# Kernel tuning notes

Hardware: AMD Instinct MI355X
Metric: run time of the kernel (lower is better)

The kernel has to match this reference:

```python
import jax, jax.numpy as jnp
import numpy as np

B, TAPE, N, F = 128, 100000, 50000, 32

def setup_inputs() -> dict:
    key = jax.random.key(0)
    k1, k2, k3, k4 = jax.random.split(key, 4)
    tape = jax.random.normal(k1, (B, TAPE), dtype=jnp.float32)
    input_indices = jax.random.randint(k2, (N, F), 0, TAPE)
    # He init scaled by fan-in, padding slots (index==0) zeroed as in __init__
    weights = jax.random.normal(k3, (N, F), dtype=jnp.float32) * jnp.sqrt(2.0 / F)
    weights = jnp.where(input_indices == 0, 0.0, weights)
    bias = jnp.zeros((N,), dtype=jnp.float32)
    output_indices = jnp.arange(N)
    act_type = jax.random.randint(k4, (N,), 0, 2)
    return {"tape": tape, "weights": weights, "bias": bias,
            "input_indices": input_indices, "output_indices": output_indices,
            "act_type": act_type}

def reference(tape, weights, bias, input_indices, output_indices, act_type):
    # gather padded fan-in inputs: [B, N, F]
    gathered = tape[:, input_indices]
    # weighted sum over fan-in + bias: [B, N]
    x = jnp.einsum('bnf,nf->bn', gathered, weights) + bias
    # per-activation-type apply (two activation groups: relu / tanh)
    x = jnp.where(act_type == 0, jax.nn.relu(x), jnp.tanh(x))
    # scatter results back into tape
    return tape.at[:, output_indices].set(x)
```

## Files before the change

kernel.cpp:

```cpp
#include <hip/hip_runtime.h>
#include <cmath>

#define TAPE_SZ 100000
#define N_SZ    50000
#define F_SZ    32
#define B_SZ    128
#define NGRP    8
#define GSUB    16
#define NBV     128
#define NCHUNK  ((N_SZ + NBV - 1) / NBV)
#define NGATHER (NCHUNK * NGRP)
#define NTAIL   512
#define TAIL_F4 1600000

static __device__ __forceinline__ unsigned short f32_to_bf16(float f) {
    unsigned int u = __float_as_uint(f);
    u = (u + 0x7fffu + ((u >> 16) & 1u)) >> 16;
    return (unsigned short)u;
}

__global__ __launch_bounds__(256) void transpose_tape(const float* __restrict__ in,
                                                      unsigned short* __restrict__ outT) {
    __shared__ float tile[32][129];
    const int x0 = blockIdx.x * 32;
    const int tx = threadIdx.x;
    const int ty = threadIdx.y;

    #pragma unroll
    for (int yy = ty; yy < B_SZ; yy += 8)
        tile[tx][yy] = in[(size_t)yy * TAPE_SZ + x0 + tx];
    __syncthreads();

    const int tid = ty * 32 + tx;
    const int g = tid >> 5;
    const int l = tid & 31;
    unsigned short* dst = outT + ((size_t)g * TAPE_SZ + x0 + l) * GSUB;
    union { unsigned short u[8]; uint4 q; } p0, p1;
    #pragma unroll
    for (int k = 0; k < 8; ++k) {
        p0.u[k] = f32_to_bf16(tile[l][g * GSUB + k]);
        p1.u[k] = f32_to_bf16(tile[l][g * GSUB + 8 + k]);
    }
    *(uint4*)dst       = p0.q;
    *(uint4*)(dst + 8) = p1.q;
}

__global__ __launch_bounds__(256) void gather_mm(const unsigned short* __restrict__ tapeT,
                                                 const float* __restrict__ weights,
                                                 const float* __restrict__ bias,
                                                 const int*   __restrict__ in_idx,
                                                 const int*   __restrict__ out_idx,
                                                 const int*   __restrict__ act_type,
                                                 const float* __restrict__ tape,
                                                 float* __restrict__ out) {
    __shared__ int   s_idx[NBV][33];
    __shared__ float s_w[NBV][33];
    __shared__ float s_bias[NBV];
    __shared__ int   s_act[NBV];
    __shared__ int   s_oidx[NBV];
    __shared__ float s_x[GSUB][132];

    const int tid = threadIdx.x;

    if (blockIdx.x >= NGATHER) {
        const float4* src = (const float4*)tape;
        float4*       dst = (float4*)out;
        const int stride = NTAIL * 256;
        for (int i = (blockIdx.x - NGATHER) * 256 + tid; i < TAIL_F4; i += stride) {
            const int b = i / 12500;
            const int j = i - b * 12500;
            const int off = b * (TAPE_SZ / 4) + (N_SZ / 4) + j;
            dst[off] = src[off];
        }
        return;
    }

    const int g     = blockIdx.x & (NGRP - 1);
    const int chunk = blockIdx.x >> 3;
    const int n0    = chunk * NBV;
    const int nend  = min(NBV, N_SZ - n0);

    for (int t = tid; t < nend * 32; t += 256) {
        const int n = t >> 5, f = t & 31;
        s_idx[n][f] = in_idx[(size_t)n0 * 32 + t];
        s_w[n][f]   = weights[(size_t)n0 * 32 + t];
    }
    if (tid < nend) {
        s_bias[tid] = bias[n0 + tid];
        s_act[tid]  = act_type[n0 + tid];
        s_oidx[tid] = out_idx[n0 + tid];
    }
    __syncthreads();

    const int nl   = tid >> 1;
    const int half = tid & 1;
    const unsigned short* tg = tapeT + (size_t)g * TAPE_SZ * GSUB + half * 8;

    if (nl < nend) {
        float a0 = 0.f, a1 = 0.f, a2 = 0.f, a3 = 0.f, a4 = 0.f, a5 = 0.f, a6 = 0.f, a7 = 0.f;

        #pragma unroll
        for (int fo = 0; fo < 32; fo += 8) {
            int   i8[8]; float w8[8];
            #pragma unroll
            for (int j = 0; j < 8; ++j) { i8[j] = s_idx[nl][fo + j]; w8[j] = s_w[nl][fo + j]; }
            uint4 q8[8];
            #pragma unroll
            for (int j = 0; j < 8; ++j)
                q8[j] = *(const uint4*)(tg + (size_t)i8[j] * GSUB);
            #pragma unroll
            for (int j = 0; j < 8; ++j) {
                const float w = w8[j];
                a0 = fmaf(__uint_as_float(q8[j].x << 16),         w, a0);
                a1 = fmaf(__uint_as_float(q8[j].x & 0xffff0000u), w, a1);
                a2 = fmaf(__uint_as_float(q8[j].y << 16),         w, a2);
                a3 = fmaf(__uint_as_float(q8[j].y & 0xffff0000u), w, a3);
                a4 = fmaf(__uint_as_float(q8[j].z << 16),         w, a4);
                a5 = fmaf(__uint_as_float(q8[j].z & 0xffff0000u), w, a5);
                a6 = fmaf(__uint_as_float(q8[j].w << 16),         w, a6);
                a7 = fmaf(__uint_as_float(q8[j].w & 0xffff0000u), w, a7);
            }
        }

        const float bz = s_bias[nl];
        a0 += bz; a1 += bz; a2 += bz; a3 += bz; a4 += bz; a5 += bz; a6 += bz; a7 += bz;
        if (s_act[nl] == 0) {
            a0 = fmaxf(a0, 0.f); a1 = fmaxf(a1, 0.f); a2 = fmaxf(a2, 0.f); a3 = fmaxf(a3, 0.f);
            a4 = fmaxf(a4, 0.f); a5 = fmaxf(a5, 0.f); a6 = fmaxf(a6, 0.f); a7 = fmaxf(a7, 0.f);
        } else {
            a0 = tanhf(a0); a1 = tanhf(a1); a2 = tanhf(a2); a3 = tanhf(a3);
            a4 = tanhf(a4); a5 = tanhf(a5); a6 = tanhf(a6); a7 = tanhf(a7);
        }
        const int bs = half * 8;
        s_x[bs + 0][nl] = a0; s_x[bs + 1][nl] = a1; s_x[bs + 2][nl] = a2; s_x[bs + 3][nl] = a3;
        s_x[bs + 4][nl] = a4; s_x[bs + 5][nl] = a5; s_x[bs + 6][nl] = a6; s_x[bs + 7][nl] = a7;
    }
    __syncthreads();

    const int quads = (nend + 3) >> 2;
    for (int idx = tid; idx < GSUB * quads; idx += 256) {
        int bsub, j4;
        if (nend == NBV) { bsub = idx >> 5; j4 = idx & 31; }
        else             { bsub = idx / quads; j4 = idx - bsub * quads; }
        const int nq  = j4 * 4;
        const int oc0 = s_oidx[nq];
        float* orow = out + (size_t)(g * GSUB + bsub) * TAPE_SZ;
        const bool consec = (nq + 3 < nend) &&
                            (s_oidx[nq + 1] == oc0 + 1) &&
                            (s_oidx[nq + 2] == oc0 + 2) &&
                            (s_oidx[nq + 3] == oc0 + 3) && ((oc0 & 3) == 0);
        if (consec) {
            *(float4*)(orow + oc0) = make_float4(s_x[bsub][nq + 0], s_x[bsub][nq + 1],
                                                 s_x[bsub][nq + 2], s_x[bsub][nq + 3]);
        } else {
            #pragma unroll
            for (int c = 0; c < 4; ++c)
                if (nq + c < nend) orow[s_oidx[nq + c]] = s_x[bsub][nq + c];
        }
    }
}

__global__ __launch_bounds__(128) void gather_fallback(const float* __restrict__ tape,
                                                       const float* __restrict__ weights,
                                                       const float* __restrict__ bias,
                                                       const int*   __restrict__ in_idx,
                                                       const int*   __restrict__ out_idx,
                                                       const int*   __restrict__ act_type,
                                                       float* __restrict__ out) {
    const int n = blockIdx.x;
    const int b = threadIdx.x;
    float acc = 0.f;
    for (int f = 0; f < F_SZ; ++f) {
        acc += tape[(size_t)b * TAPE_SZ + in_idx[(size_t)n * F_SZ + f]] *
               weights[(size_t)n * F_SZ + f];
    }
    acc += bias[n];
    acc = (act_type[n] == 0) ? fmaxf(acc, 0.f) : tanhf(acc);
    out[(size_t)b * TAPE_SZ + out_idx[n]] = acc;
}

__global__ __launch_bounds__(256) void copy_tail_fb(const float* __restrict__ tape,
                                                    float* __restrict__ out) {
    const int n4 = (TAPE_SZ - N_SZ) / 4;
    int i = blockIdx.x * blockDim.x + threadIdx.x;
    int b = blockIdx.y;
    if (i < n4) {
        const float4* src = (const float4*)(tape + (size_t)b * TAPE_SZ + N_SZ);
        float4*       dst = (float4*)(out  + (size_t)b * TAPE_SZ + N_SZ);
        dst[i] = src[i];
    }
}

extern "C" void kernel_launch(void* const* d_in, const int* in_sizes, int n_in,
                              void* d_out, int out_size, void* d_ws, size_t ws_size,
                              hipStream_t stream) {
    const float* tape    = (const float*)d_in[0];
    const float* weights = (const float*)d_in[1];
    const float* bias    = (const float*)d_in[2];
    const int*   in_idx  = (const int*)d_in[3];
    const int*   out_idx = (const int*)d_in[4];
    const int*   act     = (const int*)d_in[5];
    float*       out     = (float*)d_out;

    const size_t need = (size_t)TAPE_SZ * B_SZ * sizeof(unsigned short);
    if (ws_size >= need) {
        unsigned short* tapeT = (unsigned short*)d_ws;
        transpose_tape<<<dim3(TAPE_SZ / 32), dim3(32, 8), 0, stream>>>(tape, tapeT);
        gather_mm<<<dim3(NGATHER + NTAIL), dim3(256), 0, stream>>>(
            tapeT, weights, bias, in_idx, out_idx, act, tape, out);
    } else {
        copy_tail_fb<<<dim3(((TAPE_SZ - N_SZ) / 4 + 255) / 256, B_SZ), 256, 0, stream>>>(tape, out);
        gather_fallback<<<dim3(N_SZ), 128, 0, stream>>>(
            tape, weights, bias, in_idx, out_idx, act, out);
    }
}
```

Measured before the change: 188.5 us.

## Halve neurons per block, split batch across four threads, pack index/weight in LDS

Each block now handles 64 neurons instead of 128, and each neuron's 16-batch group is split across four threads. Each thread does 8-byte gathers and keeps four accumulators instead of eight. Indices and weights are interleaved as int2 in shared memory, and the output staging buffer aliases that array behind an extra barrier. Launch bounds request 8 blocks per CU. Together these cut registers and LDS per block to raise occupancy and memory-level parallelism for the random gathers, at the cost of smaller per-thread loads and twice as many blocks.

```diff
diff --git a/kernel.cpp b/kernel.cpp
--- a/kernel.cpp
+++ b/kernel.cpp
@@ -7,7 +7,7 @@
 #define B_SZ    128
 #define NGRP    8
 #define GSUB    16
-#define NBV     128
+#define NBV     64
 #define NCHUNK  ((N_SZ + NBV - 1) / NBV)
 #define NGATHER (NCHUNK * NGRP)
 #define NTAIL   512
@@ -45,20 +45,19 @@
     *(uint4*)(dst + 8) = p1.q;
 }
 
-__global__ __launch_bounds__(256) void gather_mm(const unsigned short* __restrict__ tapeT,
-                                                 const float* __restrict__ weights,
-                                                 const float* __restrict__ bias,
-                                                 const int*   __restrict__ in_idx,
-                                                 const int*   __restrict__ out_idx,
-                                                 const int*   __restrict__ act_type,
-                                                 const float* __restrict__ tape,
-                                                 float* __restrict__ out) {
-    __shared__ int   s_idx[NBV][33];
-    __shared__ float s_w[NBV][33];
+__global__ __launch_bounds__(256, 8) void gather_mm(const unsigned short* __restrict__ tapeT,
+                                                    const float* __restrict__ weights,
+                                                    const float* __restrict__ bias,
+                                                    const int*   __restrict__ in_idx,
+                                                    const int*   __restrict__ out_idx,
+                                                    const int*   __restrict__ act_type,
+                                                    const float* __restrict__ tape,
+                                                    float* __restrict__ out) {
+    __shared__ int2  s_iw[NBV][33];
     __shared__ float s_bias[NBV];
     __shared__ int   s_act[NBV];
     __shared__ int   s_oidx[NBV];
-    __shared__ float s_x[GSUB][132];
+    float (*s_x)[68] = (float (*)[68])&s_iw[0][0];
 
     const int tid = threadIdx.x;
 
@@ -82,8 +81,8 @@
 
     for (int t = tid; t < nend * 32; t += 256) {
         const int n = t >> 5, f = t & 31;
-        s_idx[n][f] = in_idx[(size_t)n0 * 32 + t];
-        s_w[n][f]   = weights[(size_t)n0 * 32 + t];
+        s_iw[n][f] = make_int2(in_idx[(size_t)n0 * 32 + t],
+                               __float_as_int(weights[(size_t)n0 * 32 + t]));
     }
     if (tid < nend) {
         s_bias[tid] = bias[n0 + tid];
@@ -92,55 +91,52 @@
     }
     __syncthreads();
 
-    const int nl   = tid >> 1;
-    const int half = tid & 1;
-    const unsigned short* tg = tapeT + (size_t)g * TAPE_SZ * GSUB + half * 8;
-
+    const int nl = tid >> 2;
+    const int q  = tid & 3;
+    const unsigned short* tg = tapeT + (size_t)g * TAPE_SZ * GSUB + q * 4;
+
+    float a0 = 0.f, a1 = 0.f, a2 = 0.f, a3 = 0.f;
     if (nl < nend) {
-        float a0 = 0.f, a1 = 0.f, a2 = 0.f, a3 = 0.f, a4 = 0.f, a5 = 0.f, a6 = 0.f, a7 = 0.f;
-
         #pragma unroll
         for (int fo = 0; fo < 32; fo += 8) {
-            int   i8[8]; float w8[8];
-            #pragma unroll
-            for (int j = 0; j < 8; ++j) { i8[j] = s_idx[nl][fo + j]; w8[j] = s_w[nl][fo + j]; }
-            uint4 q8[8];
+            int2 iw8[8];
+            #pragma unroll
+            for (int j = 0; j < 8; ++j) iw8[j] = s_iw[nl][fo + j];
+            uint2 q8[8];
             #pragma unroll
             for (int j = 0; j < 8; ++j)
-                q8[j] = *(const uint4*)(tg + (size_t)i8[j] * GSUB);
+                q8[j] = *(const uint2*)(tg + (size_t)iw8[j].x * GSUB);
             #pragma unroll
             for (int j = 0; j < 8; ++j) {
-                const float w = w8[j];
+                const float w = __int_as_float(iw8[j].y);
                 a0 = fmaf(__uint_as_float(q8[j].x << 16),         w, a0);
                 a1 = fmaf(__uint_as_float(q8[j].x & 0xffff0000u), w, a1);
                 a2 = fmaf(__uint_as_float(q8[j].y << 16),         w, a2);
                 a3 = fmaf(__uint_as_float(q8[j].y & 0xffff0000u), w, a3);
-                a4 = fmaf(__uint_as_float(q8[j].z << 16),         w, a4);
-                a5 = fmaf(__uint_as_float(q8[j].z & 0xffff0000u), w, a5);
-                a6 = fmaf(__uint_as_float(q8[j].w << 16),         w, a6);
-                a7 = fmaf(__uint_as_float(q8[j].w & 0xffff0000u), w, a7);
             }
         }
-
         const float bz = s_bias[nl];
-        a0 += bz; a1 += bz; a2 += bz; a3 += bz; a4 += bz; a5 += bz; a6 += bz; a7 += bz;
+        a0 += bz; a1 += bz; a2 += bz; a3 += bz;
         if (s_act[nl] == 0) {
-            a0 = fmaxf(a0, 0.f); a1 = fmaxf(a1, 0.f); a2 = fmaxf(a2, 0.f); a3 = fmaxf(a3, 0.f);
-            a4 = fmaxf(a4, 0.f); a5 = fmaxf(a5, 0.f); a6 = fmaxf(a6, 0.f); a7 = fmaxf(a7, 0.f);
+            a0 = fmaxf(a0, 0.f); a1 = fmaxf(a1, 0.f);
+            a2 = fmaxf(a2, 0.f); a3 = fmaxf(a3, 0.f);
         } else {
             a0 = tanhf(a0); a1 = tanhf(a1); a2 = tanhf(a2); a3 = tanhf(a3);
-            a4 = tanhf(a4); a5 = tanhf(a5); a6 = tanhf(a6); a7 = tanhf(a7);
-        }
-        const int bs = half * 8;
-        s_x[bs + 0][nl] = a0; s_x[bs + 1][nl] = a1; s_x[bs + 2][nl] = a2; s_x[bs + 3][nl] = a3;
-        s_x[bs + 4][nl] = a4; s_x[bs + 5][nl] = a5; s_x[bs + 6][nl] = a6; s_x[bs + 7][nl] = a7;
+        }
+    }
+    __syncthreads();
+
+    if (nl < nend) {
+        const int bs = q * 4;
+        s_x[bs + 0][nl] = a0; s_x[bs + 1][nl] = a1;
+        s_x[bs + 2][nl] = a2; s_x[bs + 3][nl] = a3;
     }
     __syncthreads();
 
     const int quads = (nend + 3) >> 2;
     for (int idx = tid; idx < GSUB * quads; idx += 256) {
         int bsub, j4;
-        if (nend == NBV) { bsub = idx >> 5; j4 = idx & 31; }
+        if (nend == NBV) { bsub = idx >> 4; j4 = idx & 15; }
         else             { bsub = idx / quads; j4 = idx - bsub * quads; }
         const int nq  = j4 * 4;
         const int oc0 = s_oidx[nq];
```

After: 187.8 us. About the same (-0.4%).

## Use full-row bf16 tape layout, fuse tail copy into transpose, shrink gather blocks

Applied to the files above, without the earlier changes.

The transposed bf16 tape changes from 8 batch groups of 16 to one contiguous 128-wide row per tape column. Each gathered index then reads a contiguous 256-byte row shared by 16 threads, replacing eight separate 32-byte reads spread across groups. The tail copy of untouched tape columns moves into the transpose kernel, which already holds that data in shared memory, so the extra copy blocks in the gather kernel go away. Gather blocks now handle 16 neurons across all 128 batches, and output writes are float4 across neurons for each batch row, which gives narrower store segments per row.

```diff
diff --git a/kernel.cpp b/kernel.cpp
--- a/kernel.cpp
+++ b/kernel.cpp
@@ -5,13 +5,8 @@
 #define N_SZ    50000
 #define F_SZ    32
 #define B_SZ    128
-#define NGRP    8
-#define GSUB    16
-#define NBV     128
-#define NCHUNK  ((N_SZ + NBV - 1) / NBV)
-#define NGATHER (NCHUNK * NGRP)
-#define NTAIL   512
-#define TAIL_F4 1600000
+#define NB      16
+#define NGATHER 3125
 
 static __device__ __forceinline__ unsigned short f32_to_bf16(float f) {
     unsigned int u = __float_as_uint(f);
@@ -20,7 +15,8 @@
 }
 
 __global__ __launch_bounds__(256) void transpose_tape(const float* __restrict__ in,
-                                                      unsigned short* __restrict__ outT) {
+                                                      unsigned short* __restrict__ outT,
+                                                      float* __restrict__ out) {
     __shared__ float tile[32][129];
     const int x0 = blockIdx.x * 32;
     const int tx = threadIdx.x;
@@ -32,17 +28,23 @@
     __syncthreads();
 
     const int tid = ty * 32 + tx;
-    const int g = tid >> 5;
-    const int l = tid & 31;
-    unsigned short* dst = outT + ((size_t)g * TAPE_SZ + x0 + l) * GSUB;
-    union { unsigned short u[8]; uint4 q; } p0, p1;
+    const int oct = tid & 15;
+    const int xl0 = tid >> 4;
     #pragma unroll
-    for (int k = 0; k < 8; ++k) {
-        p0.u[k] = f32_to_bf16(tile[l][g * GSUB + k]);
-        p1.u[k] = f32_to_bf16(tile[l][g * GSUB + 8 + k]);
+    for (int xx = xl0; xx < 32; xx += 16) {
+        const float* src = &tile[xx][oct * 8];
+        union { unsigned short u[8]; uint4 q; } pk;
+        #pragma unroll
+        for (int k = 0; k < 8; ++k)
+            pk.u[k] = f32_to_bf16(src[k]);
+        *(uint4*)(outT + (size_t)(x0 + xx) * B_SZ + oct * 8) = pk.q;
     }
-    *(uint4*)dst       = p0.q;
-    *(uint4*)(dst + 8) = p1.q;
+
+    if (x0 + tx >= N_SZ) {
+        #pragma unroll
+        for (int yy = ty; yy < B_SZ; yy += 8)
+            out[(size_t)yy * TAPE_SZ + x0 + tx] = tile[tx][yy];
+    }
 }
 
 __global__ __launch_bounds__(256) void gather_mm(const unsigned short* __restrict__ tapeT,
@@ -51,111 +53,91 @@
                                                  const int*   __restrict__ in_idx,
                                                  const int*   __restrict__ out_idx,
                                                  const int*   __restrict__ act_type,
-                                                 const float* __restrict__ tape,
                                                  float* __restrict__ out) {
-    __shared__ int   s_idx[NBV][33];
-    __shared__ float s_w[NBV][33];
-    __shared__ float s_bias[NBV];
-    __shared__ int   s_act[NBV];
-    __shared__ int   s_oidx[NBV];
-    __shared__ float s_x[GSUB][132];
+    __shared__ int   s_idx[NB][33];
+    __shared__ float s_w[NB][33];
+    __shared__ float s_bias[NB];
+    __shared__ int   s_act[NB];
+    __shared__ int   s_oidx[NB];
+    __shared__ float s_x[NB][132];
 
     const int tid = threadIdx.x;
+    const int n0 = blockIdx.x * NB;
 
-    if (blockIdx.x >= NGATHER) {
-        const float4* src = (const float4*)tape;
-        float4*       dst = (float4*)out;
-        const int stride = NTAIL * 256;
-        for (int i = (blockIdx.x - NGATHER) * 256 + tid; i < TAIL_F4; i += stride) {
-            const int b = i / 12500;
-            const int j = i - b * 12500;
-            const int off = b * (TAPE_SZ / 4) + (N_SZ / 4) + j;
-            dst[off] = src[off];
-        }
-        return;
-    }
-
-    const int g     = blockIdx.x & (NGRP - 1);
-    const int chunk = blockIdx.x >> 3;
-    const int n0    = chunk * NBV;
-    const int nend  = min(NBV, N_SZ - n0);
-
-    for (int t = tid; t < nend * 32; t += 256) {
+    #pragma unroll
+    for (int t = tid; t < NB * 32; t += 256) {
         const int n = t >> 5, f = t & 31;
         s_idx[n][f] = in_idx[(size_t)n0 * 32 + t];
         s_w[n][f]   = weights[(size_t)n0 * 32 + t];
     }
-    if (tid < nend) {
+    if (tid < NB) {
         s_bias[tid] = bias[n0 + tid];
         s_act[tid]  = act_type[n0 + tid];
         s_oidx[tid] = out_idx[n0 + tid];
     }
     __syncthreads();
 
-    const int nl   = tid >> 1;
-    const int half = tid & 1;
-    const unsigned short* tg = tapeT + (size_t)g * TAPE_SZ * GSUB + half * 8;
+    const int nl = tid >> 4;
+    const int bx = tid & 15;
+    float a0 = 0.f, a1 = 0.f, a2 = 0.f, a3 = 0.f, a4 = 0.f, a5 = 0.f, a6 = 0.f, a7 = 0.f;
 
-    if (nl < nend) {
-        float a0 = 0.f, a1 = 0.f, a2 = 0.f, a3 = 0.f, a4 = 0.f, a5 = 0.f, a6 = 0.f, a7 = 0.f;
+    #pragma unroll
+    for (int fo = 0; fo < 32; fo += 8) {
+        int   i8[8]; float w8[8];
+        #pragma unroll
+        for (int j = 0; j < 8; ++j) { i8[j] = s_idx[nl][fo + j]; w8[j] = s_w[nl][fo + j]; }
+        uint4 q8[8];
+        #pragma unroll
+        for (int j = 0; j < 8; ++j)
+            q8[j] = *(const uint4*)(tapeT + (size_t)i8[j] * B_SZ + bx * 8);
+        #pragma unroll
+        for (int j = 0; j < 8; ++j) {
+            const float w = w8[j];
+            a0 = fmaf(__uint_as_float(q8[j].x << 16),         w, a0);
+            a1 = fmaf(__uint_as_float(q8[j].x & 0xffff0000u), w, a1);
+            a2 = fmaf(__uint_as_float(q8[j].y << 16),         w, a2);
+            a3 = fmaf(__uint_as_float(q8[j].y & 0xffff0000u), w, a3);
+            a4 = fmaf(__uint_as_float(q8[j].z << 16),         w, a4);
+            a5 = fmaf(__uint_as_float(q8[j].z & 0xffff0000u), w, a5);
+            a6 = fmaf(__uint_as_float(q8[j].w << 16),         w, a6);
+            a7 = fmaf(__uint_as_float(q8[j].w & 0xffff0000u), w, a7);
+        }
+    }
 
-        #pragma unroll
-        for (int fo = 0; fo < 32; fo += 8) {
-            int   i8[8]; float w8[8];
-            #pragma unroll
-            for (int j = 0; j < 8; ++j) { i8[j] = s_idx[nl][fo + j]; w8[j] = s_w[nl][fo + j]; }
-            uint4 q8[8];
-            #pragma unroll
-            for (int j = 0; j < 8; ++j)
-                q8[j] = *(const uint4*)(tg + (size_t)i8[j] * GSUB);
-            #pragma unroll
-            for (int j = 0; j < 8; ++j) {
-                const float w = w8[j];
-                a0 = fmaf(__uint_as_float(q8[j].x << 16),         w, a0);
-                a1 = fmaf(__uint_as_float(q8[j].x & 0xffff0000u), w, a1);
-                a2 = fmaf(__uint_as_float(q8[j].y << 16),         w, a2);
-                a3 = fmaf(__uint_as_float(q8[j].y & 0xffff0000u), w, a3);
-                a4 = fmaf(__uint_as_float(q8[j].z << 16),         w, a4);
-                a5 = fmaf(__uint_as_float(q8[j].z & 0xffff0000u), w, a5);
-                a6 = fmaf(__uint_as_float(q8[j].w << 16),         w, a6);
-                a7 = fmaf(__uint_as_float(q8[j].w & 0xffff0000u), w, a7);
-            }
-        }
-
-        const float bz = s_bias[nl];
-        a0 += bz; a1 += bz; a2 += bz; a3 += bz; a4 += bz; a5 += bz; a6 += bz; a7 += bz;
-        if (s_act[nl] == 0) {
-            a0 = fmaxf(a0, 0.f); a1 = fmaxf(a1, 0.f); a2 = fmaxf(a2, 0.f); a3 = fmaxf(a3, 0.f);
-            a4 = fmaxf(a4, 0.f); a5 = fmaxf(a5, 0.f); a6 = fmaxf(a6, 0.f); a7 = fmaxf(a7, 0.f);
-        } else {
-            a0 = tanhf(a0); a1 = tanhf(a1); a2 = tanhf(a2); a3 = tanhf(a3);
-            a4 = tanhf(a4); a5 = tanhf(a5); a6 = tanhf(a6); a7 = tanhf(a7);
-        }
-        const int bs = half * 8;
-        s_x[bs + 0][nl] = a0; s_x[bs + 1][nl] = a1; s_x[bs + 2][nl] = a2; s_x[bs + 3][nl] = a3;
-        s_x[bs + 4][nl] = a4; s_x[bs + 5][nl] = a5; s_x[bs + 6][nl] = a6; s_x[bs + 7][nl] = a7;
+    const float bz = s_bias[nl];
+    a0 += bz; a1 += bz; a2 += bz; a3 += bz; a4 += bz; a5 += bz; a6 += bz; a7 += bz;
+    if (s_act[nl] == 0) {
+        a0 = fmaxf(a0, 0.f); a1 = fmaxf(a1, 0.f); a2 = fmaxf(a2, 0.f); a3 = fmaxf(a3, 0.f);
+        a4 = fmaxf(a4, 0.f); a5 = fmaxf(a5, 0.f); a6 = fmaxf(a6, 0.f); a7 = fmaxf(a7, 0.f);
+    } else {
+        a0 = tanhf(a0); a1 = tanhf(a1); a2 = tanhf(a2); a3 = tanhf(a3);
+        a4 = tanhf(a4); a5 = tanhf(a5); a6 = tanhf(a6); a7 = tanhf(a7);
+    }
+    {
+        const int b8 = bx * 8;
+        s_x[nl][b8 + 0] = a0; s_x[nl][b8 + 1] = a1; s_x[nl][b8 + 2] = a2; s_x[nl][b8 + 3] = a3;
+        s_x[nl][b8 + 4] = a4; s_x[nl][b8 + 5] = a5; s_x[nl][b8 + 6] = a6; s_x[nl][b8 + 7] = a7;
     }
     __syncthreads();
 
-    const int quads = (nend + 3) >> 2;
-    for (int idx = tid; idx < GSUB * quads; idx += 256) {
-        int bsub, j4;
-        if (nend == NBV) { bsub = idx >> 5; j4 = idx & 31; }
-        else             { bsub = idx / quads; j4 = idx - bsub * quads; }
-        const int nq  = j4 * 4;
-        const int oc0 = s_oidx[nq];
-        float* orow = out + (size_t)(g * GSUB + bsub) * TAPE_SZ;
-        const bool consec = (nq + 3 < nend) &&
-                            (s_oidx[nq + 1] == oc0 + 1) &&
-                            (s_oidx[nq + 2] == oc0 + 2) &&
-                            (s_oidx[nq + 3] == oc0 + 3) && ((oc0 & 3) == 0);
+    const int g  = tid >> 6;
+    const int b0 = tid & 63;
+    const int oc0 = s_oidx[g * 4];
+    const bool consec = (s_oidx[g * 4 + 1] == oc0 + 1) &&
+                        (s_oidx[g * 4 + 2] == oc0 + 2) &&
+                        (s_oidx[g * 4 + 3] == oc0 + 3) && ((oc0 & 3) == 0);
+    #pragma unroll
+    for (int rep = 0; rep < 2; ++rep) {
+        const int b = b0 + rep * 64;
+        const float4 v = make_float4(s_x[g * 4 + 0][b], s_x[g * 4 + 1][b],
+                                     s_x[g * 4 + 2][b], s_x[g * 4 + 3][b]);
         if (consec) {
-            *(float4*)(orow + oc0) = make_float4(s_x[bsub][nq + 0], s_x[bsub][nq + 1],
-                                                 s_x[bsub][nq + 2], s_x[bsub][nq + 3]);
+            *(float4*)(out + (size_t)b * TAPE_SZ + oc0) = v;
         } else {
-            #pragma unroll
-            for (int c = 0; c < 4; ++c)
-                if (nq + c < nend) orow[s_oidx[nq + c]] = s_x[bsub][nq + c];
+            out[(size_t)b * TAPE_SZ + s_oidx[g * 4 + 0]] = v.x;
+            out[(size_t)b * TAPE_SZ + s_oidx[g * 4 + 1]] = v.y;
+            out[(size_t)b * TAPE_SZ + s_oidx[g * 4 + 2]] = v.z;
+            out[(size_t)b * TAPE_SZ + s_oidx[g * 4 + 3]] = v.w;
         }
     }
 }
@@ -205,9 +187,9 @@
     const size_t need = (size_t)TAPE_SZ * B_SZ * sizeof(unsigned short);
     if (ws_size >= need) {
         unsigned short* tapeT = (unsigned short*)d_ws;
-        transpose_tape<<<dim3(TAPE_SZ / 32), dim3(32, 8), 0, stream>>>(tape, tapeT);
-        gather_mm<<<dim3(NGATHER + NTAIL), dim3(256), 0, stream>>>(
-            tapeT, weights, bias, in_idx, out_idx, act, tape, out);
+        transpose_tape<<<dim3(TAPE_SZ / 32), dim3(32, 8), 0, stream>>>(tape, tapeT, out);
+        gather_mm<<<dim3(NGATHER), dim3(256), 0, stream>>>(
+            tapeT, weights, bias, in_idx, out_idx, act, out);
     } else {
         copy_tail_fb<<<dim3(((TAPE_SZ - N_SZ) / 4 + 255) / 256, B_SZ), 256, 0, stream>>>(tape, out);
         gather_fallback<<<dim3(N_SZ), 128, 0, stream>>>(
```

Measured after the change: 170.4 us. 1.11x faster.
